# Performance work log

Measured on AMD Instinct MI355X. Metric: run time of the kernel, lower is better.

## Reference

```python
import jax, jax.numpy as jnp
import numpy as np

N_NODES = 50000
N_EDGES = 400000
C_IN = 256
HID = 512
C_OUT = 128
N_GRAPHS = 64
BN_EPS = 1e-5


def setup_inputs() -> dict:
    key = jax.random.key(0)
    ks = jax.random.split(key, 18)
    s_in = 1.0 / np.sqrt(C_IN)
    s_h = 1.0 / np.sqrt(HID)
    inp = {
        'x': jax.random.normal(ks[0], (N_NODES, C_IN), jnp.float32),
        'edge_index': jax.random.randint(ks[1], (2, N_EDGES), 0, N_NODES, jnp.int32).astype(jnp.int64),
        'batch': jnp.sort(jax.random.randint(ks[2], (N_NODES,), 0, N_GRAPHS, jnp.int32)).astype(jnp.int64),
        'enc_w': jax.random.normal(ks[3], (C_IN, HID), jnp.float32) * s_in,
        'enc_b': jax.random.normal(ks[4], (HID,), jnp.float32) * s_in,
        'conv_w0': jax.random.normal(ks[5], (2, HID, HID), jnp.float32) * s_h,
        'conv_b0': jax.random.normal(ks[6], (2, HID), jnp.float32) * s_h,
        'bn0_g': jax.random.uniform(ks[7], (2, HID), jnp.float32, 0.5, 1.5),
        'bn0_b': jax.random.normal(ks[8], (2, HID), jnp.float32) * 0.1,
        'conv_w1': jax.random.normal(ks[9], (2, HID, HID), jnp.float32) * s_h,
        'conv_b1': jax.random.normal(ks[10], (2, HID), jnp.float32) * s_h,
        'bn1_g': jax.random.uniform(ks[11], (2, HID), jnp.float32, 0.5, 1.5),
        'bn1_b': jax.random.normal(ks[12], (2, HID), jnp.float32) * 0.1,
        'lin_w': jax.random.normal(ks[13], (HID, HID), jnp.float32) * s_h,
        'lin_b': jax.random.normal(ks[14], (HID,), jnp.float32) * s_h,
        'clf_w': jax.random.normal(ks[15], (HID, C_OUT), jnp.float32) * s_h,
        'clf_b': jax.random.normal(ks[16], (C_OUT,), jnp.float32) * s_h,
    }
    return inp


def _bn_eval(h, gamma, beta):
    # BatchNorm1d in eval mode with default buffers: running_mean=0, running_var=1
    return h * (gamma / jnp.sqrt(1.0 + BN_EPS)) + beta


def reference(x, edge_index, batch, enc_w, enc_b, conv_w0, conv_b0, bn0_g, bn0_b,
              conv_w1, conv_b1, bn1_g, bn1_b, lin_w, lin_b, clf_w, clf_b):
    src, dst = edge_index[0], edge_index[1]
    n = x.shape[0]
    # encoder (gbn output is dead code in the original forward; omitted)
    x = x @ enc_w + enc_b  # [N, HID]
    # GIN_Net: 2 GINConv layers, eps=0, sum aggregation, MLP = Lin-BN-ReLU-Lin-BN
    for i in range(2):
        agg = jax.ops.segment_sum(x[src], dst, num_segments=n)  # scatter-add of neighbor feats
        h = x + agg  # (1 + eps) * x + aggr, eps = 0
        h = h @ conv_w0[i] + conv_b0[i]
        h = jax.nn.relu(_bn_eval(h, bn0_g[i], bn0_b[i]))
        h = h @ conv_w1[i] + conv_b1[i]
        h = _bn_eval(h, bn1_g[i], bn1_b[i])
        # inter-layer relu (dropout p=0 / eval -> identity); skipped after last layer
        x = h if i == 1 else jax.nn.relu(h)
    # global mean pooling over graphs
    sums = jax.ops.segment_sum(x, batch, num_segments=N_GRAPHS)  # [G, HID]
    counts = jax.ops.segment_sum(jnp.ones((n,), x.dtype), batch, num_segments=N_GRAPHS)
    pooled = sums / jnp.maximum(counts, 1.0)[:, None]
    g = jax.nn.gelu(pooled @ lin_w + lin_b, approximate=False)
    # dropout(0.5) identity in eval mode
    return g @ clf_w + clf_b  # [G, C_OUT]
```

## Files before the change

### kernel.cpp

```cpp
#include <hip/hip_runtime.h>
#include <hip/hip_bf16.h>
#include <stdint.h>

#define NN 50000
#define M_PAD 50176
#define NE 400000
#define CIN 256
#define KF 320
#define HID 512
#define COUT 128
#define NG 64
#define SCAN_NB ((NN + 255) / 256)
#define CVT_NB (NN * CIN / 4 / 256)
#define HIST_NB ((NE + 255) / 256)
#define GEMM_NWG 392

typedef short bf16x8 __attribute__((ext_vector_type(8)));
typedef float f32x4 __attribute__((ext_vector_type(4)));

__device__ inline float bf2f(unsigned short u) {
    union { unsigned int i; float f; } v; v.i = ((unsigned int)u) << 16; return v.f;
}
__device__ inline unsigned short f2bf(float f) {
    union { float f; unsigned int u; } v; v.f = f;
    unsigned int r = v.u + 0x7fffu + ((v.u >> 16) & 1u);
    return (unsigned short)(r >> 16);
}

__device__ inline void async16(const void* g, void* l) {
    __builtin_amdgcn_global_load_lds((const __attribute__((address_space(1))) void*)g,
                                     (__attribute__((address_space(3))) void*)l, 16, 0, 0);
}


__global__ void k_prep0(const float* __restrict__ xf, unsigned short* __restrict__ xbf,
                        const int* __restrict__ dst, int* __restrict__ indeg) {
    int b = blockIdx.x;
    if (b < CVT_NB) {
        int i = b * 256 + threadIdx.x;
        float4 v = ((const float4*)xf)[i];
        ushort4 o;
        o.x = f2bf(v.x); o.y = f2bf(v.y); o.z = f2bf(v.z); o.w = f2bf(v.w);
        ((ushort4*)xbf)[i] = o;
    } else {
        int i = (b - CVT_NB) * 256 + threadIdx.x;
        if (i < NE) atomicAdd(&indeg[dst[i]], 1);
    }
}

__global__ void k_transpose2(const float* __restrict__ s0, const float* __restrict__ s1,
                             unsigned short* __restrict__ d0, unsigned short* __restrict__ d1) {
    const float* in = blockIdx.z ? s1 : s0;
    unsigned short* out = blockIdx.z ? d1 : d0;
    __shared__ float tile[32][33];
    int bx = blockIdx.x * 32, by = blockIdx.y * 32;
    int tx = threadIdx.x & 31, ty = threadIdx.x >> 5;
    for (int i = 0; i < 32; i += 8)
        tile[ty + i][tx] = in[(size_t)(by + ty + i) * HID + bx + tx];
    __syncthreads();
    for (int i = 0; i < 32; i += 8)
        out[(size_t)(bx + ty + i) * HID + by + tx] = f2bf(tile[tx][ty + i]);
}

__global__ void k_fuse_w0(const float* __restrict__ enc_w, const float* __restrict__ enc_b,
                          const float* __restrict__ W0, unsigned short* __restrict__ WfT) {
    int n = blockIdx.x;
    __shared__ float col[HID];
    for (int j = threadIdx.x; j < HID; j += 256) col[j] = W0[(size_t)j * HID + n];
    __syncthreads();
    int k = threadIdx.x;
    float acc = 0.f;
    for (int j = 0; j < HID; j++) acc += enc_w[(size_t)k * HID + j] * col[j];
    WfT[(size_t)n * KF + k] = f2bf(acc);
    if (k == 0) {
        float v = 0.f;
        for (int j = 0; j < HID; j++) v += enc_b[j] * col[j];
        WfT[(size_t)n * KF + 256] = f2bf(v);
    }
    if (k >= 1 && k < 64) WfT[(size_t)n * KF + 256 + k] = 0;
}

__global__ void k_affine_bounds(const float* __restrict__ enc_b,
                                const float* __restrict__ cb0, const float* __restrict__ bg0, const float* __restrict__ bb0,
                                const float* __restrict__ cb1, const float* __restrict__ bg1, const float* __restrict__ bb1,
                                float* __restrict__ scale, float* __restrict__ shift,
                                const int* __restrict__ batch, int* __restrict__ bounds) {
    int c = threadIdx.x;
    const float inv = 0.9999950000374997f;
    scale[c] = 1.f; shift[c] = enc_b[c];
    for (int l = 0; l < 2; l++) {
        float s0 = bg0[l * HID + c] * inv;
        scale[(1 + 2 * l) * HID + c] = s0;
        shift[(1 + 2 * l) * HID + c] = cb0[l * HID + c] * s0 + bb0[l * HID + c];
        float s1 = bg1[l * HID + c] * inv;
        scale[(2 + 2 * l) * HID + c] = s1;
        shift[(2 + 2 * l) * HID + c] = cb1[l * HID + c] * s1 + bb1[l * HID + c];
    }
    if (c <= NG) {
        int lo = 0, hi = NN;
        while (lo < hi) { int mid = (lo + hi) >> 1; if (batch[mid] < c) lo = mid + 1; else hi = mid; }
        bounds[c] = lo;
    }
}


__global__ void k_scan1(const int* __restrict__ indeg, int* __restrict__ local,
                        int* __restrict__ blocksum, int n) {
    __shared__ int s[256];
    int t = threadIdx.x;
    int i = blockIdx.x * 256 + t;
    int v = (i < n) ? indeg[i] : 0;
    s[t] = v;
    __syncthreads();
    for (int d = 1; d < 256; d <<= 1) {
        int u = (t >= d) ? s[t - d] : 0;
        __syncthreads();
        s[t] += u;
        __syncthreads();
    }
    if (i < n) local[i] = s[t] - v;
    if (t == 255) blocksum[blockIdx.x] = s[255];
}

__global__ void k_scan3(const int* __restrict__ local, const int* __restrict__ blocksum,
                        const int* __restrict__ indeg, int* __restrict__ off,
                        int* __restrict__ cursor, int n) {
    __shared__ int s[256];
    int t = threadIdx.x;
    s[t] = (t < blockIdx.x && t < SCAN_NB) ? blocksum[t] : 0;
    __syncthreads();
    for (int d = 128; d > 0; d >>= 1) {
        if (t < d) s[t] += s[t + d];
        __syncthreads();
    }
    int ps = s[0];
    int i = blockIdx.x * 256 + t;
    if (i < n) {
        int o = local[i] + ps;
        off[i] = o;
        cursor[i] = o;
        if (i == n - 1) off[n] = o + indeg[i];
    }
}

__global__ void k_fill(const int* __restrict__ src, const int* __restrict__ dst,
                       int* __restrict__ cursor, int* __restrict__ csr, int n) {
    int i = blockIdx.x * blockDim.x + threadIdx.x;
    if (i < n) {
        int p = atomicAdd(&cursor[dst[i]], 1);
        csr[p] = src[i];
    }
}


__global__ void k_aggregate0(const unsigned short* __restrict__ x, const int* __restrict__ off,
                             const int* __restrict__ csr, unsigned short* __restrict__ z) {
    int wid = (int)((blockIdx.x * blockDim.x + threadIdx.x) >> 6);
    if (wid >= NN) return;
    int lane = threadIdx.x & 63;
    const uint2* xr = (const uint2*)x;
    uint2 v = xr[(size_t)wid * 64 + lane];
    float acc[4];
    {
        unsigned short* p = (unsigned short*)&v;
        for (int i = 0; i < 4; i++) acc[i] = bf2f(p[i]);
    }
    int e0 = off[wid], e1 = off[wid + 1];
    int e = e0;
    for (; e + 7 < e1; e += 8) {
        uint2 vv[8];
#pragma unroll
        for (int q = 0; q < 8; q++) vv[q] = xr[(size_t)csr[e + q] * 64 + lane];
#pragma unroll
        for (int q = 0; q < 8; q++) {
            unsigned short* p = (unsigned short*)&vv[q];
#pragma unroll
            for (int i = 0; i < 4; i++) acc[i] += bf2f(p[i]);
        }
    }
    for (; e < e1; e++) {
        int u = csr[e];
        uint2 vu = xr[(size_t)u * 64 + lane];
        unsigned short* p = (unsigned short*)&vu;
#pragma unroll
        for (int i = 0; i < 4; i++) acc[i] += bf2f(p[i]);
    }
    uint2 o;
    unsigned short* po = (unsigned short*)&o;
    for (int i = 0; i < 4; i++) po[i] = f2bf(acc[i]);
    uint2* zr = (uint2*)z;
    zr[(size_t)wid * 80 + lane] = o;
    if (lane < 16) {
        uint2 ex; ex.x = 0; ex.y = 0;
        if (lane == 0) ex.x = (unsigned)f2bf((float)(1 + e1 - e0));
        zr[(size_t)wid * 80 + 64 + lane] = ex;
    }
}


__global__ void k_aggregate(const unsigned short* __restrict__ x, const int* __restrict__ off,
                            const int* __restrict__ csr, unsigned short* __restrict__ h) {
    int wid = (int)((blockIdx.x * blockDim.x + threadIdx.x) >> 6);
    if (wid >= NN) return;
    int lane = threadIdx.x & 63;
    const uint4* xr = (const uint4*)x;
    uint4 v = xr[(size_t)wid * 64 + lane];
    float acc[8];
    {
        unsigned short* p = (unsigned short*)&v;
        for (int i = 0; i < 8; i++) acc[i] = bf2f(p[i]);
    }
    int e0 = off[wid], e1 = off[wid + 1];
    int e = e0;
    for (; e + 7 < e1; e += 8) {
        uint4 vv[8];
#pragma unroll
        for (int q = 0; q < 8; q++) vv[q] = xr[(size_t)csr[e + q] * 64 + lane];
#pragma unroll
        for (int q = 0; q < 8; q++) {
            unsigned short* p = (unsigned short*)&vv[q];
#pragma unroll
            for (int i = 0; i < 8; i++) acc[i] += bf2f(p[i]);
        }
    }
    for (; e < e1; e++) {
        int u = csr[e];
        uint4 vu = xr[(size_t)u * 64 + lane];
        unsigned short* p = (unsigned short*)&vu;
#pragma unroll
        for (int i = 0; i < 8; i++) acc[i] += bf2f(p[i]);
    }
    uint4 o;
    unsigned short* po = (unsigned short*)&o;
    for (int i = 0; i < 8; i++) po[i] = f2bf(acc[i]);
    ((uint4*)h)[(size_t)wid * 64 + lane] = o;
}


template <int RELU, int NSTEPS>
__global__ __launch_bounds__(512, 2) void k_gemm(const unsigned short* __restrict__ A,
                                                 const unsigned short* __restrict__ WT,
                                                 const float* __restrict__ scale,
                                                 const float* __restrict__ shift,
                                                 unsigned short* __restrict__ out) {
    constexpr int K = NSTEPS * 64;
    __shared__ char lds[131072];
    const int tid = threadIdx.x, w = tid >> 6, lane = tid & 63;
    const int wr = w >> 2, wc = w & 3;
    const int lr = lane & 15, lh = lane >> 4;

    int orig = blockIdx.x;
    int wgid = (orig & 7) * 49 + (orig >> 3);
    int tile_m = (wgid >> 1) * 256;
    int n0 = (wgid & 1) * 256;

    const unsigned short* gA[4];
    const unsigned short* gB[4];
    int ldsoff[4];
#pragma unroll
    for (int ci = 0; ci < 4; ci++) {
        int c = w * 4 + ci;
        int f = c >> 1, kf = c & 1;
        ldsoff[ci] = c * 1024;
        gA[ci] = A + (size_t)(tile_m + f * 16 + lr) * K + kf * 32 + lh * 8;
        gB[ci] = WT + (size_t)(n0 + f * 16 + lr) * K + kf * 32 + lh * 8;
    }

    f32x4 acc[8][4];
#pragma unroll
    for (int x = 0; x < 8; x++)
#pragma unroll
        for (int y = 0; y < 4; y++) acc[x][y] = f32x4{0.f, 0.f, 0.f, 0.f};

#pragma unroll
    for (int ci = 0; ci < 4; ci++) async16(gA[ci], lds + ldsoff[ci]);
#pragma unroll
    for (int ci = 0; ci < 4; ci++) async16(gB[ci], lds + 32768 + ldsoff[ci]);
#pragma unroll
    for (int ci = 0; ci < 4; ci++) async16(gA[ci] + 64, lds + 65536 + ldsoff[ci]);
#pragma unroll
    for (int ci = 0; ci < 4; ci++) async16(gB[ci] + 64, lds + 65536 + 32768 + ldsoff[ci]);

#pragma unroll
    for (int ks = 0; ks < NSTEPS; ks++) {
        const int cur = (ks & 1) << 16;
        if (ks < NSTEPS - 1) asm volatile("s_waitcnt vmcnt(8)" ::: "memory");
        else                 asm volatile("s_waitcnt vmcnt(0)" ::: "memory");
        __builtin_amdgcn_s_barrier();
        __builtin_amdgcn_sched_barrier(0);
#pragma unroll
        for (int kf = 0; kf < 2; kf++) {
            bf16x8 a[8], bb[4];
#pragma unroll
            for (int mf = 0; mf < 8; mf++)
                a[mf] = *(const bf16x8*)(lds + cur + ((wr * 8 + mf) * 2 + kf) * 1024 + lane * 16);
#pragma unroll
            for (int nf = 0; nf < 4; nf++)
                bb[nf] = *(const bf16x8*)(lds + cur + 32768 + ((wc * 4 + nf) * 2 + kf) * 1024 + lane * 16);
#pragma unroll
            for (int mf = 0; mf < 8; mf++)
#pragma unroll
                for (int nf = 0; nf < 4; nf++)
                    acc[mf][nf] = __builtin_amdgcn_mfma_f32_16x16x32_bf16(bb[nf], a[mf], acc[mf][nf], 0, 0, 0);
        }
        __builtin_amdgcn_sched_barrier(0);
        __builtin_amdgcn_s_barrier();
        if (ks + 2 < NSTEPS) {
            int ko = (ks + 2) << 6;
#pragma unroll
            for (int ci = 0; ci < 4; ci++) async16(gA[ci] + ko, lds + cur + ldsoff[ci]);
#pragma unroll
            for (int ci = 0; ci < 4; ci++) async16(gB[ci] + ko, lds + cur + 32768 + ldsoff[ci]);
        }
    }

#pragma unroll
    for (int nf = 0; nf < 4; nf++) {
        int col = n0 + wc * 64 + nf * 16 + lh * 4;
        float4 sc = *(const float4*)&scale[col];
        float4 sh = *(const float4*)&shift[col];
#pragma unroll
        for (int mf = 0; mf < 8; mf++) {
            int row = tile_m + wr * 128 + mf * 16 + lr;
            float y0 = acc[mf][nf][0] * sc.x + sh.x;
            float y1 = acc[mf][nf][1] * sc.y + sh.y;
            float y2 = acc[mf][nf][2] * sc.z + sh.z;
            float y3 = acc[mf][nf][3] * sc.w + sh.w;
            if (RELU) {
                y0 = fmaxf(y0, 0.f); y1 = fmaxf(y1, 0.f);
                y2 = fmaxf(y2, 0.f); y3 = fmaxf(y3, 0.f);
            }
            ushort4 pk;
            pk.x = f2bf(y0); pk.y = f2bf(y1); pk.z = f2bf(y2); pk.w = f2bf(y3);
            *(ushort4*)(out + (size_t)row * HID + col) = pk;
        }
    }
}


__global__ void k_pool(const unsigned short* __restrict__ x, const int* __restrict__ bounds,
                       float* __restrict__ pooled) {
    int g = blockIdx.x, s = blockIdx.y, t = threadIdx.x;
    int b0 = bounds[g], b1 = bounds[g + 1];
    int len = b1 - b0;
    int r0 = b0 + (int)((long long)len * s / 8);
    int r1 = b0 + (int)((long long)len * (s + 1) / 8);
    float acc = 0.f;
    for (int r = r0; r < r1; r++) acc += bf2f(x[(size_t)r * HID + t]);
    if (r1 > r0) atomicAdd(&pooled[g * HID + t], acc);
}

__global__ void k_tail(const float* __restrict__ pooledSum, const int* __restrict__ bounds,
                       const float* __restrict__ W1, const float* __restrict__ scale,
                       const float* __restrict__ shift,
                       const float* __restrict__ lin_w, const float* __restrict__ lin_b,
                       const float* __restrict__ clf_w, const float* __restrict__ clf_b,
                       float* __restrict__ out) {
    int g = blockIdx.x, t = threadIdx.x;
    __shared__ float r0[HID], r1[HID], r2[HID];
    int cnt = bounds[g + 1] - bounds[g];
    float invc = 1.f / fmaxf((float)cnt, 1.f);
    r0[t] = pooledSum[g * HID + t] * invc;
    __syncthreads();
    {
        float acc = 0.f;
        for (int k = 0; k < HID; k++) acc += r0[k] * W1[(size_t)k * HID + t];
        r1[t] = acc * scale[t] + shift[t];
    }
    __syncthreads();
    {
        float acc = lin_b[t];
        for (int k = 0; k < HID; k++) acc += r1[k] * lin_w[(size_t)k * HID + t];
        r2[t] = 0.5f * acc * (1.f + erff(acc * 0.7071067811865475f));
    }
    __syncthreads();
    if (t < COUT) {
        float acc = clf_b[t];
        for (int k = 0; k < HID; k++) acc += r2[k] * clf_w[(size_t)k * COUT + t];
        out[g * COUT + t] = acc;
    }
}


extern "C" void kernel_launch(void* const* d_in, const int* in_sizes, int n_in,
                              void* d_out, int out_size, void* d_ws, size_t ws_size,
                              hipStream_t stream) {
    const float* x_f32   = (const float*)d_in[0];
    const int*   ei      = (const int*)d_in[1];
    const int*   batch   = (const int*)d_in[2];
    const float* enc_w   = (const float*)d_in[3];
    const float* enc_b   = (const float*)d_in[4];
    const float* conv_w0 = (const float*)d_in[5];
    const float* conv_b0 = (const float*)d_in[6];
    const float* bn0_g   = (const float*)d_in[7];
    const float* bn0_b   = (const float*)d_in[8];
    const float* conv_w1 = (const float*)d_in[9];
    const float* conv_b1 = (const float*)d_in[10];
    const float* bn1_g   = (const float*)d_in[11];
    const float* bn1_b   = (const float*)d_in[12];
    const float* lin_w   = (const float*)d_in[13];
    const float* lin_b   = (const float*)d_in[14];
    const float* clf_w   = (const float*)d_in[15];
    const float* clf_b   = (const float*)d_in[16];
    const int* srcp = ei;
    const int* dstp = ei + NE;

    char* ws = (char*)d_ws;
    size_t o = 0;
    auto alloc = [&](size_t b) { size_t r = o; o += (b + 255) & ~(size_t)255; return r; };
    unsigned short* buf0 = (unsigned short*)(ws + alloc((size_t)M_PAD * HID * 2));
    unsigned short* buf1 = (unsigned short*)(ws + alloc((size_t)M_PAD * HID * 2));
    unsigned short* buf2 = (unsigned short*)(ws + alloc((size_t)M_PAD * HID * 2));
    unsigned short* xbf  = buf0;
    unsigned short* zbuf = buf2;
    unsigned short* WfT  = (unsigned short*)(ws + alloc((size_t)HID * KF * 2));
    unsigned short* c0T  = (unsigned short*)(ws + alloc((size_t)HID * HID * 2));
    unsigned short* c1T  = (unsigned short*)(ws + alloc((size_t)HID * HID * 2));
    float* aff_scale = (float*)(ws + alloc(5 * HID * 4));
    float* aff_shift = (float*)(ws + alloc(5 * HID * 4));
    int* indeg  = (int*)(ws + alloc((size_t)NN * 4));
    int* off    = (int*)(ws + alloc((size_t)(NN + 1) * 4));
    int* cursor = (int*)(ws + alloc((size_t)NN * 4));
    int* csr    = (int*)(ws + alloc((size_t)NE * 4));
    int* scan_local = (int*)(ws + alloc((size_t)NN * 4));
    int* scan_bsum  = (int*)(ws + alloc((size_t)256 * 4));
    int* bounds = (int*)(ws + alloc((size_t)(NG + 1) * 4));
    float* pooledSum = (float*)(ws + alloc((size_t)NG * HID * 4));
    (void)ws_size; (void)n_in; (void)in_sizes; (void)out_size;

    hipMemsetAsync(indeg, 0, (size_t)NN * 4, stream);
    hipMemsetAsync(pooledSum, 0, (size_t)NG * HID * 4, stream);

    k_prep0<<<CVT_NB + HIST_NB, 256, 0, stream>>>(x_f32, xbf, dstp, indeg);
    k_fuse_w0<<<HID, 256, 0, stream>>>(enc_w, enc_b, conv_w0, WfT);
    k_transpose2<<<dim3(16, 16, 2), 256, 0, stream>>>(conv_w0 + HID * HID, conv_w1, c0T, c1T);
    k_affine_bounds<<<1, 512, 0, stream>>>(enc_b, conv_b0, bn0_g, bn0_b, conv_b1, bn1_g, bn1_b,
                                           aff_scale, aff_shift, batch, bounds);

    k_scan1<<<SCAN_NB, 256, 0, stream>>>(indeg, scan_local, scan_bsum, NN);
    k_scan3<<<SCAN_NB, 256, 0, stream>>>(scan_local, scan_bsum, indeg, off, cursor, NN);
    k_fill<<<HIST_NB, 256, 0, stream>>>(srcp, dstp, cursor, csr, NE);

    k_aggregate0<<<(NN * 64) / 256, 256, 0, stream>>>(xbf, off, csr, zbuf);
    k_gemm<1, KF / 64><<<GEMM_NWG, 512, 0, stream>>>(zbuf, WfT,
                                                     aff_scale + 1 * HID, aff_shift + 1 * HID, buf0);
    k_gemm<1, HID / 64><<<GEMM_NWG, 512, 0, stream>>>(buf0, c1T,
                                                      aff_scale + 2 * HID, aff_shift + 2 * HID, buf2);

    k_aggregate<<<(NN * 64) / 256, 256, 0, stream>>>(buf2, off, csr, buf1);
    k_gemm<1, HID / 64><<<GEMM_NWG, 512, 0, stream>>>(buf1, c0T,
                                                      aff_scale + 3 * HID, aff_shift + 3 * HID, buf2);

    k_pool<<<dim3(NG, 8), 512, 0, stream>>>(buf2, bounds, pooledSum);
    k_tail<<<NG, 512, 0, stream>>>(pooledSum, bounds, conv_w1 + HID * HID,
                                   aff_scale + 4 * HID, aff_shift + 4 * HID,
                                   lin_w, lin_b, clf_w, clf_b, (float*)d_out);
}
```

Before: 445.2 us.

## Restructure GEMM main loop into four-quadrant ping-pong with interleaved prefetch

Replaces the two-stage-ahead prefetch loop with a one-ahead double buffer. Global-to-LDS loads for the next K step are split into four pairs, each issued between MFMA quadrant sub-blocks. The MFMA work per step is divided into four 4x2 quadrants, each with its own LDS fragment loads, s_setprio boosting and barriers. The aim is to overlap memory traffic with matrix math and reduce register pressure from fragment arrays, at the cost of more barriers per step and a shallower prefetch distance.

```diff
diff --git a/kernel.cpp b/kernel.cpp
--- a/kernel.cpp
+++ b/kernel.cpp
@@ -276,42 +276,107 @@
     for (int ci = 0; ci < 4; ci++) async16(gA[ci], lds + ldsoff[ci]);
 #pragma unroll
     for (int ci = 0; ci < 4; ci++) async16(gB[ci], lds + 32768 + ldsoff[ci]);
-#pragma unroll
-    for (int ci = 0; ci < 4; ci++) async16(gA[ci] + 64, lds + 65536 + ldsoff[ci]);
-#pragma unroll
-    for (int ci = 0; ci < 4; ci++) async16(gB[ci] + 64, lds + 65536 + 32768 + ldsoff[ci]);
-
-#pragma unroll
-    for (int ks = 0; ks < NSTEPS; ks++) {
-        const int cur = (ks & 1) << 16;
-        if (ks < NSTEPS - 1) asm volatile("s_waitcnt vmcnt(8)" ::: "memory");
-        else                 asm volatile("s_waitcnt vmcnt(0)" ::: "memory");
+
+#pragma unroll
+    for (int t = 0; t < NSTEPS; t++) {
+        const int cur = (t & 1) << 16;
+        const int nxt = cur ^ 65536;
+        const int ko = (t + 1) << 6;
+        const bool pf = (t + 1 < NSTEPS);
+
+        bf16x8 aLo[8], aHi[8], bLo[4], bHi[4];
+
+        if (pf) {
+            async16(gA[0] + ko, lds + nxt + ldsoff[0]);
+            async16(gA[1] + ko, lds + nxt + ldsoff[1]);
+            asm volatile("s_waitcnt vmcnt(2)" ::: "memory");
+        } else {
+            asm volatile("s_waitcnt vmcnt(0)" ::: "memory");
+        }
         __builtin_amdgcn_s_barrier();
         __builtin_amdgcn_sched_barrier(0);
 #pragma unroll
-        for (int kf = 0; kf < 2; kf++) {
-            bf16x8 a[8], bb[4];
-#pragma unroll
-            for (int mf = 0; mf < 8; mf++)
-                a[mf] = *(const bf16x8*)(lds + cur + ((wr * 8 + mf) * 2 + kf) * 1024 + lane * 16);
-#pragma unroll
-            for (int nf = 0; nf < 4; nf++)
-                bb[nf] = *(const bf16x8*)(lds + cur + 32768 + ((wc * 4 + nf) * 2 + kf) * 1024 + lane * 16);
-#pragma unroll
-            for (int mf = 0; mf < 8; mf++)
-#pragma unroll
-                for (int nf = 0; nf < 4; nf++)
-                    acc[mf][nf] = __builtin_amdgcn_mfma_f32_16x16x32_bf16(bb[nf], a[mf], acc[mf][nf], 0, 0, 0);
-        }
+        for (int mf = 0; mf < 4; mf++)
+#pragma unroll
+            for (int kf = 0; kf < 2; kf++)
+                aLo[mf * 2 + kf] = *(const bf16x8*)(lds + cur + ((wr * 8 + mf) * 2 + kf) * 1024 + lane * 16);
+#pragma unroll
+        for (int nf = 0; nf < 2; nf++)
+#pragma unroll
+            for (int kf = 0; kf < 2; kf++)
+                bLo[nf * 2 + kf] = *(const bf16x8*)(lds + cur + 32768 + ((wc * 4 + nf) * 2 + kf) * 1024 + lane * 16);
+        __builtin_amdgcn_s_setprio(1);
+#pragma unroll
+        for (int kf = 0; kf < 2; kf++)
+#pragma unroll
+            for (int mf = 0; mf < 4; mf++)
+#pragma unroll
+                for (int nf = 0; nf < 2; nf++)
+                    acc[mf][nf] = __builtin_amdgcn_mfma_f32_16x16x32_bf16(bLo[nf * 2 + kf], aLo[mf * 2 + kf], acc[mf][nf], 0, 0, 0);
+        __builtin_amdgcn_s_setprio(0);
         __builtin_amdgcn_sched_barrier(0);
         __builtin_amdgcn_s_barrier();
-        if (ks + 2 < NSTEPS) {
-            int ko = (ks + 2) << 6;
-#pragma unroll
-            for (int ci = 0; ci < 4; ci++) async16(gA[ci] + ko, lds + cur + ldsoff[ci]);
-#pragma unroll
-            for (int ci = 0; ci < 4; ci++) async16(gB[ci] + ko, lds + cur + 32768 + ldsoff[ci]);
-        }
+
+        if (pf) {
+            async16(gA[2] + ko, lds + nxt + ldsoff[2]);
+            async16(gA[3] + ko, lds + nxt + ldsoff[3]);
+        }
+#pragma unroll
+        for (int nf = 0; nf < 2; nf++)
+#pragma unroll
+            for (int kf = 0; kf < 2; kf++)
+                bHi[nf * 2 + kf] = *(const bf16x8*)(lds + cur + 32768 + ((wc * 4 + 2 + nf) * 2 + kf) * 1024 + lane * 16);
+        __builtin_amdgcn_sched_barrier(0);
+        __builtin_amdgcn_s_setprio(1);
+#pragma unroll
+        for (int kf = 0; kf < 2; kf++)
+#pragma unroll
+            for (int mf = 0; mf < 4; mf++)
+#pragma unroll
+                for (int nf = 0; nf < 2; nf++)
+                    acc[mf][2 + nf] = __builtin_amdgcn_mfma_f32_16x16x32_bf16(bHi[nf * 2 + kf], aLo[mf * 2 + kf], acc[mf][2 + nf], 0, 0, 0);
+        __builtin_amdgcn_s_setprio(0);
+        __builtin_amdgcn_sched_barrier(0);
+        __builtin_amdgcn_s_barrier();
+
+        if (pf) {
+            async16(gB[0] + ko, lds + nxt + 32768 + ldsoff[0]);
+            async16(gB[1] + ko, lds + nxt + 32768 + ldsoff[1]);
+        }
+#pragma unroll
+        for (int mf = 0; mf < 4; mf++)
+#pragma unroll
+            for (int kf = 0; kf < 2; kf++)
+                aHi[mf * 2 + kf] = *(const bf16x8*)(lds + cur + ((wr * 8 + 4 + mf) * 2 + kf) * 1024 + lane * 16);
+        __builtin_amdgcn_sched_barrier(0);
+        __builtin_amdgcn_s_setprio(1);
+#pragma unroll
+        for (int kf = 0; kf < 2; kf++)
+#pragma unroll
+            for (int mf = 0; mf < 4; mf++)
+#pragma unroll
+                for (int nf = 0; nf < 2; nf++)
+                    acc[4 + mf][2 + nf] = __builtin_amdgcn_mfma_f32_16x16x32_bf16(bHi[nf * 2 + kf], aHi[mf * 2 + kf], acc[4 + mf][2 + nf], 0, 0, 0);
+        __builtin_amdgcn_s_setprio(0);
+        __builtin_amdgcn_sched_barrier(0);
+        __builtin_amdgcn_s_barrier();
+
+        if (pf) {
+            async16(gB[2] + ko, lds + nxt + 32768 + ldsoff[2]);
+            async16(gB[3] + ko, lds + nxt + 32768 + ldsoff[3]);
+        }
+        __builtin_amdgcn_sched_barrier(0);
+        __builtin_amdgcn_s_setprio(1);
+#pragma unroll
+        for (int kf = 0; kf < 2; kf++)
+#pragma unroll
+            for (int mf = 0; mf < 4; mf++)
+#pragma unroll
+                for (int nf = 0; nf < 2; nf++)
+                    acc[4 + mf][nf] = __builtin_amdgcn_mfma_f32_16x16x32_bf16(bLo[nf * 2 + kf], aHi[mf * 2 + kf], acc[4 + mf][nf], 0, 0, 0);
+        __builtin_amdgcn_s_setprio(0);
+        __builtin_amdgcn_sched_barrier(0);
+        __builtin_amdgcn_s_barrier();
     }
 
 #pragma unroll
```

Measured after the change: 444.0 us (median of 2 runs). About the same (-0.3%).

## Shrink GEMM tile to 256x128 and use triple-buffered LDS with early prefetch

Applied to the files above, without the earlier changes.

Changes the GEMM workgroup tile from 256x256 to 256x128, which doubles the grid to 784 workgroups and halves the accumulators per wave. It switches from double to triple LDS buffering so the prefetch two steps ahead can be issued right after the barrier, and it drops the second barrier per k-step. The aim is better occupancy and wave balance across CUs plus more overlap of loads with MFMA. In exchange, A-tile loads are duplicated across more workgroups and each k-step does less MFMA work, and 144KB of LDS likely limits the kernel to one workgroup per CU.

```diff
diff --git a/kernel.cpp b/kernel.cpp
--- a/kernel.cpp
+++ b/kernel.cpp
@@ -13,7 +13,7 @@
 #define SCAN_NB ((NN + 255) / 256)
 #define CVT_NB (NN * CIN / 4 / 256)
 #define HIST_NB ((NE + 255) / 256)
-#define GEMM_NWG 392
+#define GEMM_NWG 784
 
 typedef short bf16x8 __attribute__((ext_vector_type(8)));
 typedef float f32x4 __attribute__((ext_vector_type(4)));
@@ -244,74 +244,80 @@
                                                  const float* __restrict__ shift,
                                                  unsigned short* __restrict__ out) {
     constexpr int K = NSTEPS * 64;
-    __shared__ char lds[131072];
+    constexpr int BUF = 49152;
+    __shared__ char lds[147456];
     const int tid = threadIdx.x, w = tid >> 6, lane = tid & 63;
-    const int wr = w >> 2, wc = w & 3;
+    const int wr = w & 3, wc = w >> 2;
     const int lr = lane & 15, lh = lane >> 4;
 
     int orig = blockIdx.x;
-    int wgid = (orig & 7) * 49 + (orig >> 3);
-    int tile_m = (wgid >> 1) * 256;
-    int n0 = (wgid & 1) * 256;
+    int wgid = (orig & 7) * 98 + (orig >> 3);
+    int tile_m = (wgid >> 2) * 256;
+    int n0 = (wgid & 3) * 128;
 
     const unsigned short* gA[4];
-    const unsigned short* gB[4];
-    int ldsoff[4];
+    int ldsA[4];
 #pragma unroll
     for (int ci = 0; ci < 4; ci++) {
         int c = w * 4 + ci;
-        int f = c >> 1, kf = c & 1;
-        ldsoff[ci] = c * 1024;
-        gA[ci] = A + (size_t)(tile_m + f * 16 + lr) * K + kf * 32 + lh * 8;
-        gB[ci] = WT + (size_t)(n0 + f * 16 + lr) * K + kf * 32 + lh * 8;
-    }
-
-    f32x4 acc[8][4];
-#pragma unroll
-    for (int x = 0; x < 8; x++)
+        ldsA[ci] = c * 1024;
+        gA[ci] = A + (size_t)(tile_m + (c >> 1) * 16 + lr) * K + (c & 1) * 32 + lh * 8;
+    }
+    const unsigned short* gB[2];
+    int ldsB[2];
+#pragma unroll
+    for (int ci = 0; ci < 2; ci++) {
+        int c = w * 2 + ci;
+        ldsB[ci] = 32768 + c * 1024;
+        gB[ci] = WT + (size_t)(n0 + (c >> 1) * 16 + lr) * K + (c & 1) * 32 + lh * 8;
+    }
+
+    f32x4 acc[4][4];
+#pragma unroll
+    for (int x = 0; x < 4; x++)
 #pragma unroll
         for (int y = 0; y < 4; y++) acc[x][y] = f32x4{0.f, 0.f, 0.f, 0.f};
 
 #pragma unroll
-    for (int ci = 0; ci < 4; ci++) async16(gA[ci], lds + ldsoff[ci]);
-#pragma unroll
-    for (int ci = 0; ci < 4; ci++) async16(gB[ci], lds + 32768 + ldsoff[ci]);
-#pragma unroll
-    for (int ci = 0; ci < 4; ci++) async16(gA[ci] + 64, lds + 65536 + ldsoff[ci]);
-#pragma unroll
-    for (int ci = 0; ci < 4; ci++) async16(gB[ci] + 64, lds + 65536 + 32768 + ldsoff[ci]);
-
-#pragma unroll
-    for (int ks = 0; ks < NSTEPS; ks++) {
-        const int cur = (ks & 1) << 16;
-        if (ks < NSTEPS - 1) asm volatile("s_waitcnt vmcnt(8)" ::: "memory");
-        else                 asm volatile("s_waitcnt vmcnt(0)" ::: "memory");
+    for (int ci = 0; ci < 4; ci++) async16(gA[ci], lds + ldsA[ci]);
+#pragma unroll
+    for (int ci = 0; ci < 2; ci++) async16(gB[ci], lds + ldsB[ci]);
+#pragma unroll
+    for (int ci = 0; ci < 4; ci++) async16(gA[ci] + 64, lds + BUF + ldsA[ci]);
+#pragma unroll
+    for (int ci = 0; ci < 2; ci++) async16(gB[ci] + 64, lds + BUF + ldsB[ci]);
+
+#pragma unroll
+    for (int j = 0; j < NSTEPS; j++) {
+        const int cur = (j % 3) * BUF;
+        if (j < NSTEPS - 1) asm volatile("s_waitcnt vmcnt(6)" ::: "memory");
+        else                asm volatile("s_waitcnt vmcnt(0)" ::: "memory");
         __builtin_amdgcn_s_barrier();
         __builtin_amdgcn_sched_barrier(0);
+        if (j + 2 < NSTEPS) {
+            const int nb = ((j + 2) % 3) * BUF;
+            const int ko = (j + 2) << 6;
+#pragma unroll
+            for (int ci = 0; ci < 4; ci++) async16(gA[ci] + ko, lds + nb + ldsA[ci]);
+#pragma unroll
+            for (int ci = 0; ci < 2; ci++) async16(gB[ci] + ko, lds + nb + ldsB[ci]);
+        }
 #pragma unroll
         for (int kf = 0; kf < 2; kf++) {
-            bf16x8 a[8], bb[4];
-#pragma unroll
-            for (int mf = 0; mf < 8; mf++)
-                a[mf] = *(const bf16x8*)(lds + cur + ((wr * 8 + mf) * 2 + kf) * 1024 + lane * 16);
+            bf16x8 a[4], bb[4];
+#pragma unroll
+            for (int mf = 0; mf < 4; mf++)
+                a[mf] = *(const bf16x8*)(lds + cur + ((wr * 4 + mf) * 2 + kf) * 1024 + lane * 16);
 #pragma unroll
             for (int nf = 0; nf < 4; nf++)
                 bb[nf] = *(const bf16x8*)(lds + cur + 32768 + ((wc * 4 + nf) * 2 + kf) * 1024 + lane * 16);
 #pragma unroll
-            for (int mf = 0; mf < 8; mf++)
+            for (int mf = 0; mf < 4; mf++)
 #pragma unroll
                 for (int nf = 0; nf < 4; nf++)
                     acc[mf][nf] = __builtin_amdgcn_mfma_f32_16x16x32_bf16(bb[nf], a[mf], acc[mf][nf], 0, 0, 0);
         }
         __builtin_amdgcn_sched_barrier(0);
-        __builtin_amdgcn_s_barrier();
-        if (ks + 2 < NSTEPS) {
-            int ko = (ks + 2) << 6;
-#pragma unroll
-            for (int ci = 0; ci < 4; ci++) async16(gA[ci] + ko, lds + cur + ldsoff[ci]);
-#pragma unroll
-            for (int ci = 0; ci < 4; ci++) async16(gB[ci] + ko, lds + cur + 32768 + ldsoff[ci]);
-        }
     }
 
 #pragma unroll
@@ -320,8 +326,8 @@
         float4 sc = *(const float4*)&scale[col];
         float4 sh = *(const float4*)&shift[col];
 #pragma unroll
-        for (int mf = 0; mf < 8; mf++) {
-            int row = tile_m + wr * 128 + mf * 16 + lr;
+        for (int mf = 0; mf < 4; mf++) {
+            int row = tile_m + wr * 64 + mf * 16 + lr;
             float y0 = acc[mf][nf][0] * sc.x + sh.x;
             float y1 = acc[mf][nf][1] * sc.y + sh.y;
             float y2 = acc[mf][nf][2] * sc.z + sh.z;
```

Result: slower. 472.7 us (+6.2%).
